# Optimization experiments

Measured on AMD Instinct MI355X. Metric: run time of the kernel, lower is better.

## Reference

```python
import jax, jax.numpy as jnp
import numpy as np

EMBED_DIM = 768
NUM_HEADS = 12
HEAD_DIM = EMBED_DIM // NUM_HEADS
B, T = 2, 2048


def setup_inputs() -> dict:
    key = jax.random.key(0)
    ks = jax.random.split(key, 11)
    s = 1.0 / np.sqrt(EMBED_DIM)
    return {
        "query": jax.random.normal(ks[0], (B, T, EMBED_DIM), jnp.float32),
        "key_in": jax.random.normal(ks[1], (B, T, EMBED_DIM), jnp.float32),
        "value": jax.random.normal(ks[2], (B, T, EMBED_DIM), jnp.float32),
        "Wq": jax.random.uniform(ks[3], (EMBED_DIM, EMBED_DIM), jnp.float32, -s, s),
        "bq": jnp.zeros((EMBED_DIM,), jnp.float32),
        "Wk": jax.random.uniform(ks[4], (EMBED_DIM, EMBED_DIM), jnp.float32, -s, s),
        "bk": jnp.zeros((EMBED_DIM,), jnp.float32),
        "Wv": jax.random.uniform(ks[5], (EMBED_DIM, EMBED_DIM), jnp.float32, -s, s),
        "bv": jnp.zeros((EMBED_DIM,), jnp.float32),
        "Wo": jax.random.uniform(ks[6], (EMBED_DIM, EMBED_DIM), jnp.float32, -s, s),
        "bo": jnp.zeros((EMBED_DIM,), jnp.float32),
    }


def reference(query, key_in, value, Wq, bq, Wk, bk, Wv, bv, Wo, bo):
    b, t, _ = query.shape

    def split_heads(x):  # [B,T,E] -> [B,H,T,Dh]
        return x.reshape(b, t, NUM_HEADS, HEAD_DIM).transpose(0, 2, 1, 3)

    Q = split_heads(query @ Wq + bq)
    K = split_heads(key_in @ Wk + bk)
    V = split_heads(value @ Wv + bv)

    scores = jnp.einsum("bhqd,bhkd->bhqk", Q, K) / np.sqrt(HEAD_DIM).astype(np.float32)
    attn = jax.nn.softmax(scores, axis=-1)
    out = jnp.einsum("bhqk,bhkd->bhqd", attn, V)  # [B,H,T,Dh]
    out = out.transpose(0, 2, 1, 3).reshape(b, t, EMBED_DIM)
    return out @ Wo + bo
```

## Files before the change

kernel.cpp:

```cpp
#include <hip/hip_runtime.h>
#include <math.h>

typedef __attribute__((ext_vector_type(4))) float  floatx4;
typedef __attribute__((ext_vector_type(8))) short  short8;
typedef __attribute__((ext_vector_type(4))) short  short4v;
typedef __attribute__((ext_vector_type(8))) __bf16 bf16x8;

#define E_DIM 768
#define T_DIM 2048
#define N_B   2
#define N_H   12
#define H_D   64
#define M_TOT 4096

#define Q_SCALE 0.1803368801111204f

__device__ __forceinline__ unsigned short f32_to_bf16(float f) {
  unsigned int u = __float_as_uint(f);
  u += 0x7fffu + ((u >> 16) & 1u);
  return (unsigned short)(u >> 16);
}

__device__ __forceinline__ void lds_barrier() {
  asm volatile("s_waitcnt lgkmcnt(0)\n\ts_barrier" ::: "memory");
}

__device__ __forceinline__ void gload_lds16(const unsigned short* g, unsigned short* l) {
  __builtin_amdgcn_global_load_lds(
      (const __attribute__((address_space(1))) unsigned int*)(const void*)g,
      (__attribute__((address_space(3))) unsigned int*)(void*)l, 16, 0, 0);
}

__global__ __launch_bounds__(256) void convert_x(const float* __restrict__ q,
                                                 const float* __restrict__ k,
                                                 const float* __restrict__ v,
                                                 unsigned short* __restrict__ Xb) {
  const int z = blockIdx.y;
  const float* src = (z == 0) ? q : (z == 1) ? k : v;
  size_t idx = ((size_t)blockIdx.x * 256 + threadIdx.x) * 4;
  float4 val = *reinterpret_cast<const float4*>(&src[idx]);
  short4v o;
  o[0] = (short)f32_to_bf16(val.x);
  o[1] = (short)f32_to_bf16(val.y);
  o[2] = (short)f32_to_bf16(val.z);
  o[3] = (short)f32_to_bf16(val.w);
  *reinterpret_cast<short4v*>(&Xb[(size_t)z * M_TOT * E_DIM + idx]) = o;
}

__global__ __launch_bounds__(256) void transpose_w(const float* __restrict__ W,
                                                   unsigned short* __restrict__ Wt) {
  __shared__ float tile[32][33];
  int k0 = blockIdx.x * 32, n0 = blockIdx.y * 32;
  int tx = threadIdx.x & 31, ty = threadIdx.x >> 5;
  for (int i = 0; i < 4; i++)
    tile[ty + i * 8][tx] = W[(size_t)(k0 + ty + i * 8) * E_DIM + n0 + tx];
  __syncthreads();
  for (int i = 0; i < 4; i++)
    Wt[(size_t)(n0 + ty + i * 8) * E_DIM + k0 + tx] = f32_to_bf16(tile[tx][ty + i * 8]);
}

__global__ __launch_bounds__(256) void gemm_qkv(const unsigned short* __restrict__ Xb,
                                                const unsigned short* __restrict__ WtAll,
                                                const float* __restrict__ bq,
                                                const float* __restrict__ bk,
                                                const float* __restrict__ bv,
                                                unsigned short* __restrict__ outQKV) {
  __shared__ unsigned short As[128 * 32];
  __shared__ unsigned short Bs[128 * 32];

  const int z = blockIdx.z;
  const unsigned short* A = Xb + (size_t)z * M_TOT * E_DIM;
  const float* bias = (z == 0) ? bq : (z == 1) ? bk : bv;
  const unsigned short* W = WtAll + (size_t)z * E_DIM * E_DIM;
  unsigned short* out = outQKV + (size_t)z * M_TOT * E_DIM;
  const float scale = (z == 0) ? Q_SCALE : 1.0f;

  const int tid = threadIdx.x;
  const int lane = tid & 63, wv = tid >> 6;
  const int m15 = lane & 15, quad = lane >> 4;
  const int wm = (wv & 1) * 64, wn = (wv >> 1) * 64;
  const int m0 = blockIdx.x * 128, n0 = blockIdx.y * 128;

  floatx4 acc[4][4] = {};
  const int srow = lane >> 2, scol = (lane & 3) * 8;

  for (int k0 = 0; k0 < E_DIM; k0 += 32) {
    for (int cc = 0; cc < 2; cc++) {
      int c = wv * 2 + cc;
      gload_lds16(&A[(size_t)(m0 + c * 16 + srow) * E_DIM + k0 + scol], &As[c * 512]);
      gload_lds16(&W[(size_t)(n0 + c * 16 + srow) * E_DIM + k0 + scol], &Bs[c * 512]);
    }
    __syncthreads();
    bf16x8 af[4], bfr[4];
    for (int i = 0; i < 4; i++)
      af[i] = *reinterpret_cast<const bf16x8*>(&As[(wm + i * 16 + m15) * 32 + quad * 8]);
    for (int j = 0; j < 4; j++)
      bfr[j] = *reinterpret_cast<const bf16x8*>(&Bs[(wn + j * 16 + m15) * 32 + quad * 8]);
    for (int i = 0; i < 4; i++)
      for (int j = 0; j < 4; j++)
        acc[i][j] = __builtin_amdgcn_mfma_f32_16x16x32_bf16(af[i], bfr[j], acc[i][j], 0, 0, 0);
    __syncthreads();
  }

  for (int i = 0; i < 4; i++)
    for (int j = 0; j < 4; j++) {
      int gn = n0 + wn + j * 16 + m15;
      int h = gn >> 6, d = gn & 63;
      float bso = bias[gn];
      for (int r = 0; r < 4; r++) {
        int gm = m0 + wm + i * 16 + quad * 4 + r;
        int bb = gm >> 11, tt = gm & 2047;
        float v = (acc[i][j][r] + bso) * scale;
        out[(((size_t)bb * N_H + h) * T_DIM + tt) * H_D + d] = f32_to_bf16(v);
      }
    }
}

__global__ __launch_bounds__(256) void transpose_v(const unsigned short* __restrict__ Vg_all,
                                                   unsigned short* __restrict__ VT) {
  __shared__ unsigned short tile[64 * 72];
  const int t0 = blockIdx.x * 64, h = blockIdx.y, bb = blockIdx.z;
  const unsigned short* Vg = Vg_all + (((size_t)bb * N_H + h) * T_DIM) * H_D;
  unsigned short* VTh = VT + (((size_t)bb * N_H + h) * H_D) * T_DIM;
  const int tid = threadIdx.x;
  const int tloc = tid & 63, d0 = (tid >> 6) * 16;

  short8 r0 = *reinterpret_cast<const short8*>(&Vg[(size_t)(t0 + tloc) * H_D + d0]);
  short8 r1 = *reinterpret_cast<const short8*>(&Vg[(size_t)(t0 + tloc) * H_D + d0 + 8]);
#pragma unroll
  for (int j = 0; j < 8; j++) {
    tile[(d0 + j) * 72 + tloc] = (unsigned short)r0[j];
    tile[(d0 + 8 + j) * 72 + tloc] = (unsigned short)r1[j];
  }
  __syncthreads();
  const int d = tid >> 2, ts = (tid & 3) * 16;
  short8 w0 = *reinterpret_cast<const short8*>(&tile[d * 72 + ts]);
  short8 w1 = *reinterpret_cast<const short8*>(&tile[d * 72 + ts + 8]);
  *reinterpret_cast<short8*>(&VTh[(size_t)d * T_DIM + t0 + ts]) = w0;
  *reinterpret_cast<short8*>(&VTh[(size_t)d * T_DIM + t0 + ts + 8]) = w1;
}

__global__ __launch_bounds__(256) void attn(const unsigned short* __restrict__ QKV,
                                            const unsigned short* __restrict__ VT,
                                            unsigned short* __restrict__ ctx) {
  __shared__ unsigned short QPs[64 * 72];
  __shared__ unsigned short Ks[2][64 * 72];
  __shared__ unsigned short Vs[2][64 * 72];

  const int qt = blockIdx.x, h = blockIdx.y, bb = blockIdx.z;
  const size_t headoff = (((size_t)bb * N_H + h) * T_DIM) * H_D;
  const unsigned short* Qg = QKV + headoff;
  const unsigned short* Kg = QKV + (size_t)M_TOT * E_DIM + headoff;
  const unsigned short* VTg = VT + (((size_t)bb * N_H + h) * H_D) * T_DIM;

  const int tid = threadIdx.x, lane = tid & 63, wv = tid >> 6;
  const int m15 = lane & 15, quad = lane >> 4;
  const int q0 = qt * 64;
  const int rs = tid >> 3, cs = (tid & 7) * 8;

  for (int p = 0; p < 2; p++)
    *reinterpret_cast<short8*>(&QPs[(p * 32 + rs) * 72 + cs]) =
        *reinterpret_cast<const short8*>(&Qg[(size_t)(q0 + p * 32 + rs) * H_D + cs]);

  short8 kreg[2], vreg[2];
  for (int p = 0; p < 2; p++) {
    kreg[p] = *reinterpret_cast<const short8*>(&Kg[(size_t)(p * 32 + rs) * H_D + cs]);
    vreg[p] = *reinterpret_cast<const short8*>(&VTg[(size_t)(p * 32 + rs) * T_DIM + cs]);
  }

  lds_barrier();

  bf16x8 aq[2];
  aq[0] = *reinterpret_cast<const bf16x8*>(&QPs[(wv * 16 + m15) * 72 + 0 + quad * 8]);
  aq[1] = *reinterpret_cast<const bf16x8*>(&QPs[(wv * 16 + m15) * 72 + 32 + quad * 8]);

  for (int p = 0; p < 2; p++) {
    *reinterpret_cast<short8*>(&Ks[0][(p * 32 + rs) * 72 + cs]) = kreg[p];
    *reinterpret_cast<short8*>(&Vs[0][(p * 32 + rs) * 72 + cs]) = vreg[p];
  }
  for (int p = 0; p < 2; p++) {
    kreg[p] = *reinterpret_cast<const short8*>(&Kg[(size_t)(64 + p * 32 + rs) * H_D + cs]);
    vreg[p] = *reinterpret_cast<const short8*>(&VTg[(size_t)(p * 32 + rs) * T_DIM + 64 + cs]);
  }

  floatx4 o[4] = {};
  floatx4 lacc = {};
  const short8 ones_s = {0x3f80, 0x3f80, 0x3f80, 0x3f80, 0x3f80, 0x3f80, 0x3f80, 0x3f80};
  const bf16x8 onesb = __builtin_bit_cast(bf16x8, ones_s);
  unsigned short* Pw = &QPs[wv * 16 * 72];
  const int swz_r = ((m15 >> 2) & 3) << 3;

  for (int kt = 0; kt < 32; kt++) {
    const int cur = kt & 1, nxt = cur ^ 1;
    lds_barrier();
    if (kt + 1 < 32) {
      for (int p = 0; p < 2; p++) {
        *reinterpret_cast<short8*>(&Ks[nxt][(p * 32 + rs) * 72 + cs]) = kreg[p];
        *reinterpret_cast<short8*>(&Vs[nxt][(p * 32 + rs) * 72 + cs]) = vreg[p];
      }
      if (kt + 2 < 32)
        for (int p = 0; p < 2; p++) {
          kreg[p] = *reinterpret_cast<const short8*>(&Kg[(size_t)((kt + 2) * 64 + p * 32 + rs) * H_D + cs]);
          vreg[p] = *reinterpret_cast<const short8*>(&VTg[(size_t)(p * 32 + rs) * T_DIM + (kt + 2) * 64 + cs]);
        }
    }

    floatx4 s[4] = {};
    for (int kk = 0; kk < 2; kk++)
      for (int j = 0; j < 4; j++) {
        bf16x8 b = *reinterpret_cast<const bf16x8*>(&Ks[cur][(j * 16 + m15) * 72 + kk * 32 + quad * 8]);
        s[j] = __builtin_amdgcn_mfma_f32_16x16x32_bf16(aq[kk], b, s[j], 0, 0, 0);
      }

    for (int j = 0; j < 4; j++)
      for (int r = 0; r < 4; r++) {
        float pv = exp2f(s[j][r]);
        Pw[(quad * 4 + r) * 72 + ((j * 16 + m15) ^ (quad << 3))] = f32_to_bf16(pv);
      }
    asm volatile("s_waitcnt lgkmcnt(0)" ::: "memory");

    for (int kk = 0; kk < 2; kk++) {
      bf16x8 a = *reinterpret_cast<const bf16x8*>(&Pw[m15 * 72 + ((kk * 32 + quad * 8) ^ swz_r)]);
      lacc = __builtin_amdgcn_mfma_f32_16x16x32_bf16(a, onesb, lacc, 0, 0, 0);
      for (int j = 0; j < 4; j++) {
        bf16x8 b = *reinterpret_cast<const bf16x8*>(&Vs[cur][(j * 16 + m15) * 72 + kk * 32 + quad * 8]);
        o[j] = __builtin_amdgcn_mfma_f32_16x16x32_bf16(a, b, o[j], 0, 0, 0);
      }
    }
  }

  for (int j = 0; j < 4; j++)
    for (int r = 0; r < 4; r++) {
      int q = q0 + wv * 16 + quad * 4 + r;
      float v = o[j][r] / lacc[r];
      ctx[(size_t)(bb * T_DIM + q) * E_DIM + h * 64 + j * 16 + m15] = f32_to_bf16(v);
    }
}

__global__ __launch_bounds__(256) void gemm_out(const unsigned short* __restrict__ Actx,
                                                const unsigned short* __restrict__ Wt,
                                                const float* __restrict__ bias,
                                                float* __restrict__ out) {
  __shared__ unsigned short As[64 * 32];
  __shared__ unsigned short Bs[128 * 32];

  const int tid = threadIdx.x;
  const int lane = tid & 63, wv = tid >> 6;
  const int m15 = lane & 15, quad = lane >> 4;
  const int wm = (wv & 1) * 32, wn = (wv >> 1) * 64;
  const int m0 = blockIdx.x * 64, n0 = blockIdx.y * 128;

  floatx4 acc[2][4] = {};
  const int srow = lane >> 2, scol = (lane & 3) * 8;

  for (int k0 = 0; k0 < E_DIM; k0 += 32) {
    gload_lds16(&Actx[(size_t)(m0 + wv * 16 + srow) * E_DIM + k0 + scol], &As[wv * 512]);
    for (int cc = 0; cc < 2; cc++) {
      int c = wv * 2 + cc;
      gload_lds16(&Wt[(size_t)(n0 + c * 16 + srow) * E_DIM + k0 + scol], &Bs[c * 512]);
    }
    __syncthreads();
    bf16x8 af[2], bfr[4];
    for (int i = 0; i < 2; i++)
      af[i] = *reinterpret_cast<const bf16x8*>(&As[(wm + i * 16 + m15) * 32 + quad * 8]);
    for (int j = 0; j < 4; j++)
      bfr[j] = *reinterpret_cast<const bf16x8*>(&Bs[(wn + j * 16 + m15) * 32 + quad * 8]);
    for (int i = 0; i < 2; i++)
      for (int j = 0; j < 4; j++)
        acc[i][j] = __builtin_amdgcn_mfma_f32_16x16x32_bf16(af[i], bfr[j], acc[i][j], 0, 0, 0);
    __syncthreads();
  }

  for (int i = 0; i < 2; i++)
    for (int j = 0; j < 4; j++) {
      int gn = n0 + wn + j * 16 + m15;
      float bso = bias[gn];
      for (int r = 0; r < 4; r++) {
        int gm = m0 + wm + i * 16 + quad * 4 + r;
        out[(size_t)gm * E_DIM + gn] = acc[i][j][r] + bso;
      }
    }
}

extern "C" void kernel_launch(void* const* d_in, const int* in_sizes, int n_in,
                              void* d_out, int out_size, void* d_ws, size_t ws_size,
                              hipStream_t stream) {
  const float* query  = (const float*)d_in[0];
  const float* key_in = (const float*)d_in[1];
  const float* value  = (const float*)d_in[2];
  const float* Wq = (const float*)d_in[3];
  const float* bq = (const float*)d_in[4];
  const float* Wk = (const float*)d_in[5];
  const float* bk = (const float*)d_in[6];
  const float* Wv = (const float*)d_in[7];
  const float* bv = (const float*)d_in[8];
  const float* Wo = (const float*)d_in[9];
  const float* bo = (const float*)d_in[10];
  float* out = (float*)d_out;

  unsigned short* ws  = (unsigned short*)d_ws;
  unsigned short* Wt  = ws;
  unsigned short* Xb  = Wt + (size_t)4 * E_DIM * E_DIM;
  unsigned short* QKV = Xb + (size_t)3 * M_TOT * E_DIM;
  unsigned short* VT  = QKV + (size_t)3 * M_TOT * E_DIM;
  unsigned short* ctx = VT + (size_t)N_B * N_H * H_D * T_DIM;

  dim3 tb(256);
  convert_x<<<dim3(M_TOT * E_DIM / 1024, 3), tb, 0, stream>>>(query, key_in, value, Xb);
  transpose_w<<<dim3(24, 24), tb, 0, stream>>>(Wq, Wt + (size_t)0 * E_DIM * E_DIM);
  transpose_w<<<dim3(24, 24), tb, 0, stream>>>(Wk, Wt + (size_t)1 * E_DIM * E_DIM);
  transpose_w<<<dim3(24, 24), tb, 0, stream>>>(Wv, Wt + (size_t)2 * E_DIM * E_DIM);
  transpose_w<<<dim3(24, 24), tb, 0, stream>>>(Wo, Wt + (size_t)3 * E_DIM * E_DIM);

  gemm_qkv<<<dim3(32, 6, 3), tb, 0, stream>>>(Xb, Wt, bq, bk, bv, QKV);
  transpose_v<<<dim3(32, 12, 2), tb, 0, stream>>>(QKV + (size_t)2 * M_TOT * E_DIM, VT);
  attn<<<dim3(32, 12, 2), tb, 0, stream>>>(QKV, VT, ctx);
  gemm_out<<<dim3(64, 6), tb, 0, stream>>>(ctx, Wt + (size_t)3 * E_DIM * E_DIM, bo, out);
  (void)in_sizes; (void)n_in; (void)out_size; (void)ws_size;
}
```

Measured before the change: 215.4 us.

## Software-pipeline attention loop, overlapping PV of previous tile with QK of current

Restructures the attention inner loop so the P·V MFMAs for the previous key tile are issued alongside the QK^T MFMAs for the current tile, with probability strips double-buffered in LDS and K single-buffered. This is meant to hide exp and LDS-write latency behind matrix work. It also uses hardware exp2 and reciprocal builtins with truncating bf16 conversion of P, which slightly lowers precision, and merges the four weight-transpose launches into one. The extra LDS buffer and added barriers may change occupancy.

New measurement: 202.7 us. 1.06x faster.

```diff
diff --git a/kernel.cpp b/kernel.cpp
--- a/kernel.cpp
+++ b/kernel.cpp
@@ -15,10 +15,25 @@
 
 #define Q_SCALE 0.1803368801111204f
 
+#if __has_builtin(__builtin_amdgcn_exp2f)
+#define EXP2F(x) __builtin_amdgcn_exp2f(x)
+#else
+#define EXP2F(x) exp2f(x)
+#endif
+#if __has_builtin(__builtin_amdgcn_rcpf)
+#define RCPF(x) __builtin_amdgcn_rcpf(x)
+#else
+#define RCPF(x) (1.0f / (x))
+#endif
+
 __device__ __forceinline__ unsigned short f32_to_bf16(float f) {
   unsigned int u = __float_as_uint(f);
   u += 0x7fffu + ((u >> 16) & 1u);
   return (unsigned short)(u >> 16);
+}
+
+__device__ __forceinline__ unsigned short f32_to_bf16_trunc(float f) {
+  return (unsigned short)(__float_as_uint(f) >> 16);
 }
 
 __device__ __forceinline__ void lds_barrier() {
@@ -47,16 +62,22 @@
   *reinterpret_cast<short4v*>(&Xb[(size_t)z * M_TOT * E_DIM + idx]) = o;
 }
 
-__global__ __launch_bounds__(256) void transpose_w(const float* __restrict__ W,
-                                                   unsigned short* __restrict__ Wt) {
+__global__ __launch_bounds__(256) void transpose_w4(const float* __restrict__ W0,
+                                                    const float* __restrict__ W1,
+                                                    const float* __restrict__ W2,
+                                                    const float* __restrict__ W3,
+                                                    unsigned short* __restrict__ Wt) {
   __shared__ float tile[32][33];
+  const int z = blockIdx.z;
+  const float* W = (z == 0) ? W0 : (z == 1) ? W1 : (z == 2) ? W2 : W3;
+  unsigned short* dst = Wt + (size_t)z * E_DIM * E_DIM;
   int k0 = blockIdx.x * 32, n0 = blockIdx.y * 32;
   int tx = threadIdx.x & 31, ty = threadIdx.x >> 5;
   for (int i = 0; i < 4; i++)
     tile[ty + i * 8][tx] = W[(size_t)(k0 + ty + i * 8) * E_DIM + n0 + tx];
   __syncthreads();
   for (int i = 0; i < 4; i++)
-    Wt[(size_t)(n0 + ty + i * 8) * E_DIM + k0 + tx] = f32_to_bf16(tile[tx][ty + i * 8]);
+    dst[(size_t)(n0 + ty + i * 8) * E_DIM + k0 + tx] = f32_to_bf16(tile[tx][ty + i * 8]);
 }
 
 __global__ __launch_bounds__(256) void gemm_qkv(const unsigned short* __restrict__ Xb,
@@ -143,8 +164,9 @@
 __global__ __launch_bounds__(256) void attn(const unsigned short* __restrict__ QKV,
                                             const unsigned short* __restrict__ VT,
                                             unsigned short* __restrict__ ctx) {
-  __shared__ unsigned short QPs[64 * 72];
-  __shared__ unsigned short Ks[2][64 * 72];
+  __shared__ unsigned short Qs[64 * 72];
+  __shared__ unsigned short Sb[64 * 72];
+  __shared__ unsigned short Ks[64 * 72];
   __shared__ unsigned short Vs[2][64 * 72];
 
   const int qt = blockIdx.x, h = blockIdx.y, bb = blockIdx.z;
@@ -159,7 +181,7 @@
   const int rs = tid >> 3, cs = (tid & 7) * 8;
 
   for (int p = 0; p < 2; p++)
-    *reinterpret_cast<short8*>(&QPs[(p * 32 + rs) * 72 + cs]) =
+    *reinterpret_cast<short8*>(&Qs[(p * 32 + rs) * 72 + cs]) =
         *reinterpret_cast<const short8*>(&Qg[(size_t)(q0 + p * 32 + rs) * H_D + cs]);
 
   short8 kreg[2], vreg[2];
@@ -167,74 +189,106 @@
     kreg[p] = *reinterpret_cast<const short8*>(&Kg[(size_t)(p * 32 + rs) * H_D + cs]);
     vreg[p] = *reinterpret_cast<const short8*>(&VTg[(size_t)(p * 32 + rs) * T_DIM + cs]);
   }
-
   lds_barrier();
 
   bf16x8 aq[2];
-  aq[0] = *reinterpret_cast<const bf16x8*>(&QPs[(wv * 16 + m15) * 72 + 0 + quad * 8]);
-  aq[1] = *reinterpret_cast<const bf16x8*>(&QPs[(wv * 16 + m15) * 72 + 32 + quad * 8]);
+  aq[0] = *reinterpret_cast<const bf16x8*>(&Qs[(wv * 16 + m15) * 72 + 0 + quad * 8]);
+  aq[1] = *reinterpret_cast<const bf16x8*>(&Qs[(wv * 16 + m15) * 72 + 32 + quad * 8]);
 
   for (int p = 0; p < 2; p++) {
-    *reinterpret_cast<short8*>(&Ks[0][(p * 32 + rs) * 72 + cs]) = kreg[p];
+    *reinterpret_cast<short8*>(&Ks[(p * 32 + rs) * 72 + cs]) = kreg[p];
     *reinterpret_cast<short8*>(&Vs[0][(p * 32 + rs) * 72 + cs]) = vreg[p];
   }
   for (int p = 0; p < 2; p++) {
     kreg[p] = *reinterpret_cast<const short8*>(&Kg[(size_t)(64 + p * 32 + rs) * H_D + cs]);
     vreg[p] = *reinterpret_cast<const short8*>(&VTg[(size_t)(p * 32 + rs) * T_DIM + 64 + cs]);
   }
+  lds_barrier();
 
   floatx4 o[4] = {};
   floatx4 lacc = {};
   const short8 ones_s = {0x3f80, 0x3f80, 0x3f80, 0x3f80, 0x3f80, 0x3f80, 0x3f80, 0x3f80};
   const bf16x8 onesb = __builtin_bit_cast(bf16x8, ones_s);
-  unsigned short* Pw = &QPs[wv * 16 * 72];
-  const int swz_r = ((m15 >> 2) & 3) << 3;
-
-  for (int kt = 0; kt < 32; kt++) {
-    const int cur = kt & 1, nxt = cur ^ 1;
+  unsigned short* stripA = &Qs[wv * 16 * 72];
+  unsigned short* stripB = &Sb[wv * 16 * 72];
+
+  {
+    floatx4 s[4] = {};
+    for (int kk = 0; kk < 2; kk++)
+      for (int j = 0; j < 4; j++) {
+        bf16x8 b = *reinterpret_cast<const bf16x8*>(&Ks[(j * 16 + m15) * 72 + kk * 32 + quad * 8]);
+        s[j] = __builtin_amdgcn_mfma_f32_16x16x32_bf16(aq[kk], b, s[j], 0, 0, 0);
+      }
     lds_barrier();
-    if (kt + 1 < 32) {
+    for (int p = 0; p < 2; p++) {
+      *reinterpret_cast<short8*>(&Ks[(p * 32 + rs) * 72 + cs]) = kreg[p];
+      *reinterpret_cast<short8*>(&Vs[1][(p * 32 + rs) * 72 + cs]) = vreg[p];
+    }
+    for (int p = 0; p < 2; p++) {
+      kreg[p] = *reinterpret_cast<const short8*>(&Kg[(size_t)(128 + p * 32 + rs) * H_D + cs]);
+      vreg[p] = *reinterpret_cast<const short8*>(&VTg[(size_t)(p * 32 + rs) * T_DIM + 128 + cs]);
+    }
+    for (int j = 0; j < 4; j++)
+      for (int r = 0; r < 4; r++)
+        stripA[(quad * 4 + r) * 72 + j * 16 + m15] = f32_to_bf16_trunc(EXP2F(s[j][r]));
+  }
+
+  for (int kt = 1; kt < 32; kt++) {
+    unsigned short* sp_prev = (kt & 1) ? stripA : stripB;
+    unsigned short* sp_cur = (kt & 1) ? stripB : stripA;
+    const unsigned short* vprev = Vs[(kt - 1) & 1];
+    lds_barrier();
+
+    for (int kk = 0; kk < 2; kk++) {
+      bf16x8 a = *reinterpret_cast<const bf16x8*>(&sp_prev[m15 * 72 + kk * 32 + quad * 8]);
+      lacc = __builtin_amdgcn_mfma_f32_16x16x32_bf16(a, onesb, lacc, 0, 0, 0);
+      for (int j = 0; j < 4; j++) {
+        bf16x8 b = *reinterpret_cast<const bf16x8*>(&vprev[(j * 16 + m15) * 72 + kk * 32 + quad * 8]);
+        o[j] = __builtin_amdgcn_mfma_f32_16x16x32_bf16(a, b, o[j], 0, 0, 0);
+      }
+    }
+
+    floatx4 s[4] = {};
+    for (int kk = 0; kk < 2; kk++)
+      for (int j = 0; j < 4; j++) {
+        bf16x8 b = *reinterpret_cast<const bf16x8*>(&Ks[(j * 16 + m15) * 72 + kk * 32 + quad * 8]);
+        s[j] = __builtin_amdgcn_mfma_f32_16x16x32_bf16(aq[kk], b, s[j], 0, 0, 0);
+      }
+    lds_barrier();
+
+    if (kt < 31) {
       for (int p = 0; p < 2; p++) {
-        *reinterpret_cast<short8*>(&Ks[nxt][(p * 32 + rs) * 72 + cs]) = kreg[p];
-        *reinterpret_cast<short8*>(&Vs[nxt][(p * 32 + rs) * 72 + cs]) = vreg[p];
-      }
-      if (kt + 2 < 32)
+        *reinterpret_cast<short8*>(&Ks[(p * 32 + rs) * 72 + cs]) = kreg[p];
+        *reinterpret_cast<short8*>(&Vs[(kt + 1) & 1][(p * 32 + rs) * 72 + cs]) = vreg[p];
+      }
+      if (kt < 30)
         for (int p = 0; p < 2; p++) {
           kreg[p] = *reinterpret_cast<const short8*>(&Kg[(size_t)((kt + 2) * 64 + p * 32 + rs) * H_D + cs]);
           vreg[p] = *reinterpret_cast<const short8*>(&VTg[(size_t)(p * 32 + rs) * T_DIM + (kt + 2) * 64 + cs]);
         }
     }
 
-    floatx4 s[4] = {};
-    for (int kk = 0; kk < 2; kk++)
-      for (int j = 0; j < 4; j++) {
-        bf16x8 b = *reinterpret_cast<const bf16x8*>(&Ks[cur][(j * 16 + m15) * 72 + kk * 32 + quad * 8]);
-        s[j] = __builtin_amdgcn_mfma_f32_16x16x32_bf16(aq[kk], b, s[j], 0, 0, 0);
-      }
-
-    for (int j = 0; j < 4; j++)
-      for (int r = 0; r < 4; r++) {
-        float pv = exp2f(s[j][r]);
-        Pw[(quad * 4 + r) * 72 + ((j * 16 + m15) ^ (quad << 3))] = f32_to_bf16(pv);
-      }
-    asm volatile("s_waitcnt lgkmcnt(0)" ::: "memory");
-
-    for (int kk = 0; kk < 2; kk++) {
-      bf16x8 a = *reinterpret_cast<const bf16x8*>(&Pw[m15 * 72 + ((kk * 32 + quad * 8) ^ swz_r)]);
-      lacc = __builtin_amdgcn_mfma_f32_16x16x32_bf16(a, onesb, lacc, 0, 0, 0);
-      for (int j = 0; j < 4; j++) {
-        bf16x8 b = *reinterpret_cast<const bf16x8*>(&Vs[cur][(j * 16 + m15) * 72 + kk * 32 + quad * 8]);
-        o[j] = __builtin_amdgcn_mfma_f32_16x16x32_bf16(a, b, o[j], 0, 0, 0);
-      }
-    }
-  }
-
-  for (int j = 0; j < 4; j++)
-    for (int r = 0; r < 4; r++) {
-      int q = q0 + wv * 16 + quad * 4 + r;
-      float v = o[j][r] / lacc[r];
-      ctx[(size_t)(bb * T_DIM + q) * E_DIM + h * 64 + j * 16 + m15] = f32_to_bf16(v);
-    }
+    for (int j = 0; j < 4; j++)
+      for (int r = 0; r < 4; r++)
+        sp_cur[(quad * 4 + r) * 72 + j * 16 + m15] = f32_to_bf16_trunc(EXP2F(s[j][r]));
+  }
+
+  asm volatile("s_waitcnt lgkmcnt(0)" ::: "memory");
+  for (int kk = 0; kk < 2; kk++) {
+    bf16x8 a = *reinterpret_cast<const bf16x8*>(&stripB[m15 * 72 + kk * 32 + quad * 8]);
+    lacc = __builtin_amdgcn_mfma_f32_16x16x32_bf16(a, onesb, lacc, 0, 0, 0);
+    for (int j = 0; j < 4; j++) {
+      bf16x8 b = *reinterpret_cast<const bf16x8*>(&Vs[1][(j * 16 + m15) * 72 + kk * 32 + quad * 8]);
+      o[j] = __builtin_amdgcn_mfma_f32_16x16x32_bf16(a, b, o[j], 0, 0, 0);
+    }
+  }
+
+  for (int r = 0; r < 4; r++) {
+    float rl = RCPF(lacc[r]);
+    int q = q0 + wv * 16 + quad * 4 + r;
+    for (int j = 0; j < 4; j++)
+      ctx[(size_t)(bb * T_DIM + q) * E_DIM + h * 64 + j * 16 + m15] = f32_to_bf16(o[j][r] * rl);
+  }
 }
 
 __global__ __launch_bounds__(256) void gemm_out(const unsigned short* __restrict__ Actx,
@@ -307,10 +361,7 @@
 
   dim3 tb(256);
   convert_x<<<dim3(M_TOT * E_DIM / 1024, 3), tb, 0, stream>>>(query, key_in, value, Xb);
-  transpose_w<<<dim3(24, 24), tb, 0, stream>>>(Wq, Wt + (size_t)0 * E_DIM * E_DIM);
-  transpose_w<<<dim3(24, 24), tb, 0, stream>>>(Wk, Wt + (size_t)1 * E_DIM * E_DIM);
-  transpose_w<<<dim3(24, 24), tb, 0, stream>>>(Wv, Wt + (size_t)2 * E_DIM * E_DIM);
-  transpose_w<<<dim3(24, 24), tb, 0, stream>>>(Wo, Wt + (size_t)3 * E_DIM * E_DIM);
+  transpose_w4<<<dim3(24, 24, 4), tb, 0, stream>>>(Wq, Wk, Wv, Wo, Wt);
 
   gemm_qkv<<<dim3(32, 6, 3), tb, 0, stream>>>(Xb, Wt, bq, bk, bv, QKV);
   transpose_v<<<dim3(32, 12, 2), tb, 0, stream>>>(QKV + (size_t)2 * M_TOT * E_DIM, VT);
```
